# Performance work log

Hardware: AMD Instinct MI355X
Metric: run time of the kernel (lower is better)

## Reference

```python
import jax, jax.numpy as jnp
import numpy as np

TH, TW = 64, 64        # template_size (image shape)
OH, OW = 256, 256      # out_size
K = 3                  # spline order
PAD = 4                # hardcoded padding in module
OFF = PAD - (K + 1) // 2          # = 2
CX_OFF = (OH - TH) // 2           # centering_offset[0] = 96
CY_OFF = (OW - TW) // 2           # centering_offset[1] = 96
BATCH = 1024


def bspline3(p):
    # fast cubic B-spline basis, p: (B,) -> (B, 4)
    return jnp.stack([
        p ** 3 / 6,
        -p ** 3 / 2 + p ** 2 / 2 + p / 2 + 1.0 / 6,
        p ** 3 / 2 - p ** 2 + 2.0 / 3,
        (1 - p) ** 3 / 6,
    ], axis=-1)


def setup_inputs() -> dict:
    key = jax.random.key(0)
    k1, k2, k3 = jax.random.split(key, 3)
    coeffs = jax.random.normal(k1, (TH + 2 * PAD, TW + 2 * PAD), jnp.float32)
    x = (jax.random.normal(k2, (BATCH, 1, 1, 1), jnp.float32) - 0.5) * 10
    y = (jax.random.normal(k3, (BATCH, 1, 1, 1), jnp.float32) - 0.5) * 10
    return {"coeffs": coeffs, "x": x, "y": y}


def reference(coeffs, x, y):
    B = x.shape[0]
    # integer pixel shift (floor) and subpixel remainder
    px = jnp.floor(x[:, 0, 0, 0]).astype(jnp.int32)  # (B,)
    py = jnp.floor(y[:, 0, 0, 0]).astype(jnp.int32)  # (B,)
    sx = jnp.remainder(x[:, 0, 0, 0], 1.0)           # (B,)
    sy = jnp.remainder(y[:, 0, 0, 0], 1.0)           # (B,)

    bx = bspline3(sx)  # (B,4) basis along rows (i index)
    by = bspline3(sy)  # (B,4) basis along cols (j index)

    # (4,4,TH+1,TW+1) shifted coefficient windows
    slices = jnp.stack([
        jnp.stack([coeffs[i + OFF:i + OFF + TH + 1, j + OFF:j + OFF + TW + 1]
                   for j in range(K + 1)])
        for i in range(K + 1)])
    # blended template: (B, TH+1, TW+1)
    template = jnp.einsum('bi,bj,ijrc->brc', bx, by, slices)

    bi = jnp.arange(B)[:, None, None]

    # scatter along columns (dim 3 in torch): x_a[b, r, idx_a] = template[b, r, c]
    col = jnp.arange(TW + 1)
    idx_a = jnp.clip(col[None, None, :] + py[:, None, None] + CY_OFF + 1, 0, OW + 1)  # (B,1,TW+1)
    ri = jnp.arange(TH + 1)[None, :, None]
    x_a = jnp.zeros((B, OH + 2, OW + 2), template.dtype)
    x_a = x_a.at[bi, ri, idx_a].set(template)

    # scatter along rows (dim 2 in torch): x_b[b, idx_b, c] = x_a[b, r, c]
    row = jnp.arange(OH + 2)
    idx_b = jnp.clip(row[None, :, None] + px[:, None, None] + CX_OFF + 1, 0, OH + 1)  # (B,OH+2,1)
    ci = jnp.arange(OW + 2)[None, None, :]
    x_b = jnp.zeros_like(x_a).at[bi, idx_b, ci].set(x_a)

    return x_b[:, 1:-1, 1:-1][:, None]  # (B,1,OH,OW)
```

## Files before the change

kernel.cpp:

```cpp
#include <hip/hip_runtime.h>


#define CW 72

typedef float f4 __attribute__((ext_vector_type(4)));

__device__ __forceinline__ void st_nt(float* p, f4 v) {
    __builtin_nontemporal_store(v, reinterpret_cast<f4*>(p));
}

__global__ __launch_bounds__(256) void spline2d_fused4(
    const float* __restrict__ coeffs,
    const float* __restrict__ x,
    const float* __restrict__ y,
    float* __restrict__ out)
{
    __shared__ float rb[65][68];

    const int b = blockIdx.x;

    const float xv = x[b];
    const float yv = y[b];
    const float fx = floorf(xv), fy = floorf(yv);
    const int   R0 = (int)fx + 96;
    const int   C0 = (int)fy + 96;
    const float sx = xv - fx, sy = yv - fy;

    float wx0, wx1, wx2, wx3, wy0, wy1, wy2, wy3;
    {
        const float p = sx, p2 = p * p, p3 = p2 * p, q = 1.0f - p;
        wx0 = p3 * (1.0f / 6.0f);
        wx1 = -0.5f * p3 + 0.5f * p2 + 0.5f * p + (1.0f / 6.0f);
        wx2 = 0.5f * p3 - p2 + (2.0f / 3.0f);
        wx3 = q * q * q * (1.0f / 6.0f);
    }
    {
        const float p = sy, p2 = p * p, p3 = p2 * p, q = 1.0f - p;
        wy0 = p3 * (1.0f / 6.0f);
        wy1 = -0.5f * p3 + 0.5f * p2 + 0.5f * p + (1.0f / 6.0f);
        wy2 = 0.5f * p3 - p2 + (2.0f / 3.0f);
        wy3 = q * q * q * (1.0f / 6.0f);
    }

    const int t    = threadIdx.x;
    const int w    = t >> 6;
    const int lane = t & 63;

#pragma unroll
    for (int pass = 0; pass < 17; ++pass) {
        const int r = (pass << 2) + w;
        if (r <= 64) {
            const float* p0 = coeffs + (r + 2) * CW + 2;
            rb[r][lane] = p0[lane] * wx0 + p0[lane + CW] * wx1 +
                          p0[lane + 2 * CW] * wx2 + p0[lane + 3 * CW] * wx3;
            if (lane < 4) {
                const int k = 64 + lane;
                rb[r][k] = p0[k] * wx0 + p0[k + CW] * wx1 +
                           p0[k + 2 * CW] * wx2 + p0[k + 3 * CW] * wx3;
            }
        }
    }
    __syncthreads();

    float* __restrict__ obase = out + ((size_t)b << 16);
    const int  col4 = lane << 2;
    const int  c0   = col4 - C0;
    const bool cin  = (c0 >= -3 && c0 <= 64);
    const f4   z4   = {0.f, 0.f, 0.f, 0.f};

#pragma unroll 8
    for (int it = 0; it < 64; ++it) {
        const int row = (it << 2) + w;
        const int r   = row - R0;
        f4 v = z4;
        if ((unsigned)r <= 64u && cin) {
#pragma unroll
            for (int m = 0; m < 4; ++m) {
                const int c = c0 + m;
                if ((unsigned)c <= 64u) {
                    v[m] = rb[r][c] * wy0 + rb[r][c + 1] * wy1 +
                           rb[r][c + 2] * wy2 + rb[r][c + 3] * wy3;
                }
            }
        }
        st_nt(obase + (row << 8) + col4, v);
    }
}

extern "C" void kernel_launch(void* const* d_in, const int* in_sizes, int n_in,
                              void* d_out, int out_size, void* d_ws, size_t ws_size,
                              hipStream_t stream) {
    const float* coeffs = (const float*)d_in[0];
    const float* x      = (const float*)d_in[1];
    const float* y      = (const float*)d_in[2];
    float* out = (float*)d_out;

    const int batch = in_sizes[1];
    spline2d_fused4<<<batch, 256, 0, stream>>>(coeffs, x, y, out);
}
```

Measured before the change: 277.9 us.

## Zero output with memset and write only the 65x65 template patch

The output is now zeroed by hipMemsetAsync, and the kernel writes only the valid 65x65 patch with scalar stores, no longer writing every full 256x256 image with vector nontemporal stores. The goal is to drop the kernel's per-pixel bounds logic and let the memset engine do the bulk zero fill. The same 256 MB are still written by the memset, and the scalar patch stores are unaligned and partly rewrite lines the memset already touched. The timed region may also now include a separate memset launch.

```diff
diff --git a/kernel.cpp b/kernel.cpp
--- a/kernel.cpp
+++ b/kernel.cpp
@@ -3,13 +3,7 @@
 
 #define CW 72
 
-typedef float f4 __attribute__((ext_vector_type(4)));
-
-__device__ __forceinline__ void st_nt(float* p, f4 v) {
-    __builtin_nontemporal_store(v, reinterpret_cast<f4*>(p));
-}
-
-__global__ __launch_bounds__(256) void spline2d_fused4(
+__global__ __launch_bounds__(256) void spline2d_patch(
     const float* __restrict__ coeffs,
     const float* __restrict__ x,
     const float* __restrict__ y,
@@ -63,27 +57,27 @@
     __syncthreads();
 
     float* __restrict__ obase = out + ((size_t)b << 16);
-    const int  col4 = lane << 2;
-    const int  c0   = col4 - C0;
-    const bool cin  = (c0 >= -3 && c0 <= 64);
-    const f4   z4   = {0.f, 0.f, 0.f, 0.f};
+#pragma unroll
+    for (int it = 0; it < 17; ++it) {
+        const int r = (it << 2) + w;
+        if (r > 64) continue;
+        const int orow = R0 + r;
+        if ((unsigned)orow > 255u) continue;
+        float* __restrict__ orp = obase + (orow << 8);
 
-#pragma unroll 8
-    for (int it = 0; it < 64; ++it) {
-        const int row = (it << 2) + w;
-        const int r   = row - R0;
-        f4 v = z4;
-        if ((unsigned)r <= 64u && cin) {
-#pragma unroll
-            for (int m = 0; m < 4; ++m) {
-                const int c = c0 + m;
-                if ((unsigned)c <= 64u) {
-                    v[m] = rb[r][c] * wy0 + rb[r][c + 1] * wy1 +
-                           rb[r][c + 2] * wy2 + rb[r][c + 3] * wy3;
-                }
-            }
+        {
+            const int c  = lane;
+            const int oc = C0 + c;
+            const float v = rb[r][c] * wy0 + rb[r][c + 1] * wy1 +
+                            rb[r][c + 2] * wy2 + rb[r][c + 3] * wy3;
+            if ((unsigned)oc <= 255u) orp[oc] = v;
         }
-        st_nt(obase + (row << 8) + col4, v);
+        if (lane == 0) {
+            const int oc = C0 + 64;
+            const float v = rb[r][64] * wy0 + rb[r][65] * wy1 +
+                            rb[r][66] * wy2 + rb[r][67] * wy3;
+            if ((unsigned)oc <= 255u) orp[oc] = v;
+        }
     }
 }
 
@@ -96,5 +90,8 @@
     float* out = (float*)d_out;
 
     const int batch = in_sizes[1];
-    spline2d_fused4<<<batch, 256, 0, stream>>>(coeffs, x, y, out);
+    const size_t out_bytes = (size_t)batch * 256 * 256 * sizeof(float);
+
+    hipMemsetAsync(d_out, 0, out_bytes, stream);
+    spline2d_patch<<<batch, 256, 0, stream>>>(coeffs, x, y, out);
 }
```

Result: faster. 268.9 us (-3.2%).
